# Kernel optimization log

Hardware: AMD Instinct MI355X
Metric: run time of the kernel (lower is better)

## Reference

```python
import jax, jax.numpy as jnp
import numpy as np

N_NODES = 50000
N_EDGES = 600000
D_IN = 128
D_HID = 128
N_IDX = 4096


def gcn_conv(x, W, b, edge_index, num_nodes):
    """PyG GCNConv: add self loops, symmetric deg normalization, scatter-add, bias."""
    h = x @ W  # [N, D_out]
    loop = jnp.arange(num_nodes, dtype=edge_index.dtype)
    src = jnp.concatenate([edge_index[0], loop])
    dst = jnp.concatenate([edge_index[1], loop])
    deg = jax.ops.segment_sum(jnp.ones_like(dst, dtype=h.dtype), dst, num_segments=num_nodes)
    dinv = jnp.where(deg > 0, jax.lax.rsqrt(jnp.maximum(deg, 1.0)), 0.0)
    norm = dinv[src] * dinv[dst]  # [E+N]
    msgs = h[src] * norm[:, None]
    out = jax.ops.segment_sum(msgs, dst, num_segments=num_nodes)
    return out + b


def setup_inputs() -> dict:
    key = jax.random.key(0)
    ks = jax.random.split(key, 18)
    d = {
        "x": jax.random.normal(ks[0], (N_NODES, D_IN), dtype=jnp.float32),
        "syntactic_edge_index": jax.random.randint(ks[1], (2, N_EDGES), 0, N_NODES, dtype=jnp.int32),
        "sequential_edge_index": jax.random.randint(ks[2], (2, N_EDGES), 0, N_NODES, dtype=jnp.int32),
        "semantic_edge_index": jax.random.randint(ks[3], (2, N_EDGES), 0, N_NODES, dtype=jnp.int32),
        "index": jax.random.randint(ks[4], (N_IDX,), 0, N_NODES, dtype=jnp.int32),
    }
    s = 1.0 / np.sqrt(D_IN)
    names = ["syn", "seq", "sem"]
    for i, n in enumerate(names):
        d[f"w1_{n}"] = jax.random.uniform(ks[5 + i], (D_IN, D_HID), jnp.float32, -s, s)
        d[f"b1_{n}"] = jnp.zeros((D_HID,), jnp.float32)
        d[f"w2_{n}"] = jax.random.uniform(ks[8 + i], (D_HID, D_HID), jnp.float32, -s, s)
        d[f"b2_{n}"] = jnp.zeros((D_HID,), jnp.float32)
    return d


def reference(x, syntactic_edge_index, sequential_edge_index, semantic_edge_index, index,
              w1_syn, b1_syn, w1_seq, b1_seq, w1_sem, b1_sem,
              w2_syn, b2_syn, w2_seq, b2_seq, w2_sem, b2_sem):
    n = x.shape[0]
    # layer 1: three parallel GCN branches + ReLU (dropout is identity in eval mode)
    a = jax.nn.relu(gcn_conv(x, w1_syn, b1_syn, syntactic_edge_index, n))
    b = jax.nn.relu(gcn_conv(x, w1_seq, b1_seq, sequential_edge_index, n))
    c = jax.nn.relu(gcn_conv(x, w1_sem, b1_sem, semantic_edge_index, n))
    h = jnp.maximum(jnp.maximum(a, b), c)
    # layer 2
    a2 = jax.nn.relu(gcn_conv(h, w2_syn, b2_syn, syntactic_edge_index, n))
    b2 = jax.nn.relu(gcn_conv(h, w2_seq, b2_seq, sequential_edge_index, n))
    c2 = jax.nn.relu(gcn_conv(h, w2_sem, b2_sem, semantic_edge_index, n))
    out = jnp.maximum(jnp.maximum(a2, b2), c2)
    return out[index]
```

## Files before the change

kernel.cpp:

```cpp
#include <hip/hip_runtime.h>
#include <hip/hip_fp16.h>

#define NN 50000
#define NE 600000
#define NG 3
#define D  128
#define NI 4096
#define BW 1024
#define NBUCK 49
#define EPT_BIN 16
#define EPB_BIN (256 * EPT_BIN)
#define NBLK_BIN ((NE + EPB_BIN - 1) / EPB_BIN)
#define UNR 8

typedef _Float16 half8 __attribute__((ext_vector_type(8)));
typedef float floatx4 __attribute__((ext_vector_type(4)));


__global__ __launch_bounds__(256) void xcvt_kernel(const float* __restrict__ x,
    __half* __restrict__ xh, int n2) {
  int i = blockIdx.x * 256 + threadIdx.x;
  if (i >= n2) return;
  float2 v = ((const float2*)x)[i];
  ((__half2*)xh)[i] = __floats2half2_rn(v.x, v.y);
}

__global__ __launch_bounds__(256) void wcvt_kernel(
    const float* __restrict__ W0, const float* __restrict__ W1, const float* __restrict__ W2,
    const float* __restrict__ W3, const float* __restrict__ W4, const float* __restrict__ W5,
    __half* __restrict__ Wf) {
  const float* Wm[6] = {W0, W1, W2, W3, W4, W5};
  int t = blockIdx.x * 256 + threadIdx.x;
  if (t >= 6 * 2048) return;
  int mat = t >> 11;
  int fr = (t >> 6) & 31;
  int lane = t & 63;
  int tt = fr >> 2, ks = fr & 3;
  int n = tt * 16 + (lane & 15);
  int kb = ks * 32 + (lane >> 4) * 8;
  const float* W = Wm[mat];
#pragma unroll
  for (int j = 0; j < 8; j++)
    Wf[(size_t)t * 8 + j] = __float2half(W[(kb + j) * 128 + n]);
}


__global__ __launch_bounds__(256) void count_kernel(const int* __restrict__ e0,
    const int* __restrict__ e1, const int* __restrict__ e2, int* __restrict__ bucketCnt) {
  __shared__ int cnt[NBUCK];
  int g = blockIdx.y;
  const int* ei = (g == 0) ? e0 : ((g == 1) ? e1 : e2);
  int tid = threadIdx.x;
  if (tid < NBUCK) cnt[tid] = 0;
  __syncthreads();
  int base = blockIdx.x * EPB_BIN;
#pragma unroll
  for (int i = 0; i < EPT_BIN; i++) {
    int e = base + tid + i * 256;
    if (e < NE) atomicAdd(&cnt[ei[NE + e] >> 10], 1);
  }
  __syncthreads();
  if (tid < NBUCK) atomicAdd(&bucketCnt[g * NBUCK + tid], cnt[tid]);
}

__global__ void bscan_kernel(const int* __restrict__ bucketCnt, int* __restrict__ bucketBase,
                             int* __restrict__ cursor, int* __restrict__ rp) {
  int g = threadIdx.x;
  if (g >= NG) return;
  int run = 0;
  for (int b = 0; b < NBUCK; b++) {
    int c = bucketCnt[g * NBUCK + b];
    bucketBase[g * NBUCK + b] = run;
    cursor[g * NBUCK + b] = run;
    run += c;
  }
  rp[g * (NN + 1) + NN] = NE;
}

__global__ __launch_bounds__(256) void bin_kernel(const int* __restrict__ e0,
    const int* __restrict__ e1, const int* __restrict__ e2,
    int* __restrict__ cursor, unsigned int* __restrict__ binned) {
  __shared__ int cnt[NBUCK];
  __shared__ int base[NBUCK];
  int g = blockIdx.y;
  const int* ei = (g == 0) ? e0 : ((g == 1) ? e1 : e2);
  int tid = threadIdx.x;
  if (tid < NBUCK) cnt[tid] = 0;
  __syncthreads();
  int estart = blockIdx.x * EPB_BIN;
  int src[EPT_BIN], dst[EPT_BIN], rk[EPT_BIN];
#pragma unroll
  for (int i = 0; i < EPT_BIN; i++) {
    int e = estart + tid + i * 256;
    if (e < NE) {
      src[i] = ei[e];
      dst[i] = ei[NE + e];
      rk[i] = atomicAdd(&cnt[dst[i] >> 10], 1);
    } else {
      rk[i] = -1;
    }
  }
  __syncthreads();
  if (tid < NBUCK) base[tid] = (cnt[tid] > 0) ? atomicAdd(&cursor[g * NBUCK + tid], cnt[tid]) : 0;
  __syncthreads();
#pragma unroll
  for (int i = 0; i < EPT_BIN; i++) {
    if (rk[i] >= 0) {
      int b = dst[i] >> 10;
      binned[(size_t)g * NE + base[b] + rk[i]] =
          (unsigned int)src[i] | ((unsigned int)dst[i] << 16);
    }
  }
}

__global__ __launch_bounds__(256) void csr_kernel(const unsigned int* __restrict__ binned,
    const int* __restrict__ bucketBase, const int* __restrict__ bucketCnt,
    int* __restrict__ rp, int* __restrict__ col, float* __restrict__ dinv) {
  __shared__ int deg[BW];
  __shared__ int wsum[4];
  int g = blockIdx.y, b = blockIdx.x;
  int tid = threadIdx.x;
  int node0 = b * BW;
  int bb = bucketBase[g * NBUCK + b];
  int total = bucketCnt[g * NBUCK + b];
  const unsigned int* bp = binned + (size_t)g * NE + bb;
  for (int i = tid; i < BW; i += 256) deg[i] = 0;
  __syncthreads();
  for (int e = tid; e < total; e += 256) {
    unsigned int p = bp[e];
    atomicAdd(&deg[(int)(p >> 16) - node0], 1);
  }
  __syncthreads();
  int d0 = deg[tid * 4], d1 = deg[tid * 4 + 1], d2 = deg[tid * 4 + 2], d3 = deg[tid * 4 + 3];
  int s = d0 + d1 + d2 + d3;
  int lane = tid & 63;
  int incl = s;
#pragma unroll
  for (int off = 1; off < 64; off <<= 1) {
    int n = __shfl_up(incl, off, 64);
    if (lane >= off) incl += n;
  }
  if (lane == 63) wsum[tid >> 6] = incl;
  __syncthreads();
  int wbase = 0;
#pragma unroll
  for (int w = 0; w < 4; w++)
    if (w < (tid >> 6)) wbase += wsum[w];
  int ex = wbase + incl - s;
  int exs[4] = {ex, ex + d0, ex + d0 + d1, ex + d0 + d1 + d2};
  int ds[4] = {d0, d1, d2, d3};
#pragma unroll
  for (int k = 0; k < 4; k++) {
    int node = node0 + tid * 4 + k;
    if (node < NN) {
      rp[g * (NN + 1) + node] = bb + exs[k];
      dinv[g * NN + node] = rsqrtf((float)ds[k] + 1.0f);
    }
    deg[tid * 4 + k] = exs[k];
  }
  __syncthreads();
  for (int e = tid; e < total; e += 256) {
    unsigned int p = bp[e];
    int r = atomicAdd(&deg[(int)(p >> 16) - node0], 1);
    col[(size_t)g * NE + bb + r] = (int)(p & 0xffffu);
  }
}


__global__ __launch_bounds__(256) void aggf_kernel(
    const __half* __restrict__ src, const int* __restrict__ rp,
    const int* __restrict__ col, const float* __restrict__ dinv,
    const int* __restrict__ index, __half* __restrict__ tout, int nrows) {
  int w = (blockIdx.x * 256 + threadIdx.x) >> 6;
  if (w >= nrows) return;
  int lane = threadIdx.x & 63;
  int node = index ? index[w] : w;
  int d0 = lane * 2;
  float2 self = __half22float2(*(const __half2*)&src[(size_t)node * D + d0]);
  float di0 = dinv[node];
  float di1 = dinv[NN + node];
  float di2 = dinv[2 * NN + node];
  int s0 = rp[node],                e0 = rp[node + 1];
  int s1 = rp[(NN + 1) + node],     e1 = rp[(NN + 1) + node + 1];
  int s2 = rp[2 * (NN + 1) + node], e2 = rp[2 * (NN + 1) + node + 1];
  int n0 = e0 - s0, n1 = e1 - s1, n2 = e2 - s2;
  int c0 = (lane < n0) ? col[s0 + lane] : 0;
  int c1 = (lane < n1) ? col[NE + s1 + lane] : 0;
  int c2 = (lane < n2) ? col[2 * NE + s2 + lane] : 0;
  float ax0 = di0 * self.x, ay0 = di0 * self.y;
  float ax1 = di1 * self.x, ay1 = di1 * self.y;
  float ax2 = di2 * self.x, ay2 = di2 * self.y;
  int m0 = min(n0, 64), m1 = min(n1, 64), m2 = min(n2, 64);
  int mx = max(m0, max(m1, m2));
  for (int j = 0; j < mx; j += UNR) {
    float2 v0[UNR], v1[UNR], v2[UNR];
    float g0[UNR], g1[UNR], g2[UNR];
#pragma unroll
    for (int k = 0; k < UNR; k++) {
      int jk = j + k;
      int t0 = __shfl(c0, jk, 64); t0 = (jk < m0) ? t0 : node;
      int t1 = __shfl(c1, jk, 64); t1 = (jk < m1) ? t1 : node;
      int t2 = __shfl(c2, jk, 64); t2 = (jk < m2) ? t2 : node;
      g0[k] = (jk < m0) ? dinv[t0] : 0.f;
      g1[k] = (jk < m1) ? dinv[NN + t1] : 0.f;
      g2[k] = (jk < m2) ? dinv[2 * NN + t2] : 0.f;
      v0[k] = __half22float2(*(const __half2*)&src[(size_t)t0 * D + d0]);
      v1[k] = __half22float2(*(const __half2*)&src[(size_t)t1 * D + d0]);
      v2[k] = __half22float2(*(const __half2*)&src[(size_t)t2 * D + d0]);
    }
#pragma unroll
    for (int k = 0; k < UNR; k++) {
      ax0 += g0[k] * v0[k].x; ay0 += g0[k] * v0[k].y;
      ax1 += g1[k] * v1[k].x; ay1 += g1[k] * v1[k].y;
      ax2 += g2[k] * v2[k].x; ay2 += g2[k] * v2[k].y;
    }
  }
  for (int q = s0 + 64; q < e0; q += 64) {
    int nn = min(e0 - q, 64);
    int c = (lane < nn) ? col[q + lane] : 0;
    for (int j = 0; j < nn; j++) {
      int t = __shfl(c, j, 64);
      float g = dinv[t];
      float2 v = __half22float2(*(const __half2*)&src[(size_t)t * D + d0]);
      ax0 += g * v.x; ay0 += g * v.y;
    }
  }
  for (int q = s1 + 64; q < e1; q += 64) {
    int nn = min(e1 - q, 64);
    int c = (lane < nn) ? col[NE + q + lane] : 0;
    for (int j = 0; j < nn; j++) {
      int t = __shfl(c, j, 64);
      float g = dinv[NN + t];
      float2 v = __half22float2(*(const __half2*)&src[(size_t)t * D + d0]);
      ax1 += g * v.x; ay1 += g * v.y;
    }
  }
  for (int q = s2 + 64; q < e2; q += 64) {
    int nn = min(e2 - q, 64);
    int c = (lane < nn) ? col[2 * NE + q + lane] : 0;
    for (int j = 0; j < nn; j++) {
      int t = __shfl(c, j, 64);
      float g = dinv[2 * NN + t];
      float2 v = __half22float2(*(const __half2*)&src[(size_t)t * D + d0]);
      ax2 += g * v.x; ay2 += g * v.y;
    }
  }
  size_t stride = (size_t)nrows * D;
  *(__half2*)&tout[(size_t)w * D + d0]              = __floats2half2_rn(di0 * ax0, di0 * ay0);
  *(__half2*)&tout[stride + (size_t)w * D + d0]     = __floats2half2_rn(di1 * ax1, di1 * ay1);
  *(__half2*)&tout[2 * stride + (size_t)w * D + d0] = __floats2half2_rn(di2 * ax2, di2 * ay2);
}


__global__ __launch_bounds__(256) void mmf_kernel(const __half* __restrict__ A,
    const __half* __restrict__ Wf,
    const float* __restrict__ B0, const float* __restrict__ B1, const float* __restrict__ B2,
    __half* __restrict__ outh, float* __restrict__ outf, int M) {
  __shared__ _Float16 Ws[16384];
  const float* Bb[3] = {B0, B1, B2};
  const int tid = threadIdx.x;
  const int wave = tid >> 6, lane = tid & 63;
  const int wr = (wave >> 1) * 64, wc = (wave & 1) * 64;
  const int ln = lane & 15, quad = lane >> 4;
  const int row_base = blockIdx.x * 128 + wr;
  float om[4][4][4];

  for (int b = 0; b < 3; b++) {
    const __half* Wb = Wf + (size_t)b * 16384;
#pragma unroll
    for (int i = 0; i < 8; i++) {
      int id = tid + i * 256;
      *(half8*)&Ws[id * 8] = *(const half8*)&Wb[(size_t)id * 8];
    }
    __syncthreads();

    const __half* Ab = A + (size_t)b * M * D;
    float bias[4];
#pragma unroll
    for (int ct = 0; ct < 4; ct++) bias[ct] = Bb[b][wc + ct * 16 + ln];
    floatx4 acc[4][4];
#pragma unroll
    for (int rt = 0; rt < 4; rt++)
#pragma unroll
      for (int ct = 0; ct < 4; ct++)
        acc[rt][ct] = (floatx4){bias[ct], bias[ct], bias[ct], bias[ct]};

#pragma unroll
    for (int ks = 0; ks < 4; ks++) {
      half8 av[4];
#pragma unroll
      for (int rt = 0; rt < 4; rt++) {
        int r = row_base + rt * 16 + ln;
        r = (r < M) ? r : (M - 1);
        av[rt] = *(const half8*)&Ab[(size_t)r * D + ks * 32 + quad * 8];
      }
#pragma unroll
      for (int ct = 0; ct < 4; ct++) {
        int tt = (wc >> 4) + ct;
        half8 bv = *(const half8*)&Ws[((tt * 4 + ks) * 64 + lane) * 8];
#pragma unroll
        for (int rt = 0; rt < 4; rt++)
          acc[rt][ct] = __builtin_amdgcn_mfma_f32_16x16x32_f16(av[rt], bv, acc[rt][ct], 0, 0, 0);
      }
    }
#pragma unroll
    for (int rt = 0; rt < 4; rt++)
#pragma unroll
      for (int ct = 0; ct < 4; ct++)
#pragma unroll
        for (int r = 0; r < 4; r++) {
          float v = fmaxf(acc[rt][ct][r], 0.f);
          om[rt][ct][r] = (b == 0) ? v : fmaxf(om[rt][ct][r], v);
        }
    __syncthreads();
  }
#pragma unroll
  for (int rt = 0; rt < 4; rt++) {
    int m = row_base + rt * 16 + quad * 4;
#pragma unroll
    for (int r = 0; r < 4; r++) {
      if (m + r < M) {
#pragma unroll
        for (int ct = 0; ct < 4; ct++) {
          int n = wc + ct * 16 + ln;
          if (outh) outh[(size_t)(m + r) * D + n] = __float2half(om[rt][ct][r]);
          else      outf[(size_t)(m + r) * D + n] = om[rt][ct][r];
        }
      }
    }
  }
}


extern "C" void kernel_launch(void* const* d_in, const int* in_sizes, int n_in,
                              void* d_out, int out_size, void* d_ws, size_t ws_size,
                              hipStream_t stream) {
  const float* x = (const float*)d_in[0];
  const int* e0 = (const int*)d_in[1];
  const int* e1 = (const int*)d_in[2];
  const int* e2 = (const int*)d_in[3];
  const int* index = (const int*)d_in[4];
  const float* w1[3] = {(const float*)d_in[5], (const float*)d_in[9],  (const float*)d_in[13]};
  const float* b1[3] = {(const float*)d_in[6], (const float*)d_in[10], (const float*)d_in[14]};
  const float* w2[3] = {(const float*)d_in[7], (const float*)d_in[11], (const float*)d_in[15]};
  const float* b2[3] = {(const float*)d_in[8], (const float*)d_in[12], (const float*)d_in[16]};
  float* out = (float*)d_out;

  char* ws = (char*)d_ws;
  size_t o = 0;
  auto alloc = [&](size_t bytes) {
    o = (o + 255) & ~(size_t)255;
    void* p = ws + o;
    o += bytes;
    return p;
  };
  int*    rp     = (int*)alloc((size_t)NG * (NN + 1) * 4);
  int*    col    = (int*)alloc((size_t)NG * NE * 4);
  float*  dinv   = (float*)alloc((size_t)NG * NN * 4);
  int*    bcnt   = (int*)alloc((size_t)NG * NBUCK * 4);
  int*    bbase  = (int*)alloc((size_t)NG * NBUCK * 4);
  int*    bcur   = (int*)alloc((size_t)NG * NBUCK * 4);
  __half* xh     = (__half*)alloc((size_t)NN * D * 2);
  __half* Wf     = (__half*)alloc((size_t)6 * 128 * 128 * 2);
  __half* t1     = (__half*)alloc((size_t)NG * NN * D * 2);
  __half* hacc   = (__half*)alloc((size_t)NN * D * 2);
  unsigned int* binned = (unsigned int*)t1;
  __half* t2     = t1;
  (void)ws_size; (void)in_sizes; (void)n_in; (void)out_size;

  hipMemsetAsync(bcnt, 0, (size_t)NG * NBUCK * 4, stream);
  xcvt_kernel<<<(NN * D / 2 + 255) / 256, 256, 0, stream>>>(x, xh, NN * D / 2);
  wcvt_kernel<<<48, 256, 0, stream>>>(w1[0], w1[1], w1[2], w2[0], w2[1], w2[2], Wf);
  count_kernel<<<dim3(NBLK_BIN, NG), 256, 0, stream>>>(e0, e1, e2, bcnt);
  bscan_kernel<<<1, 64, 0, stream>>>(bcnt, bbase, bcur, rp);
  bin_kernel<<<dim3(NBLK_BIN, NG), 256, 0, stream>>>(e0, e1, e2, bcur, binned);
  csr_kernel<<<dim3(NBUCK, NG), 256, 0, stream>>>(binned, bbase, bcnt, rp, col, dinv);

  aggf_kernel<<<(NN * 64 + 255) / 256, 256, 0, stream>>>(xh, rp, col, dinv, nullptr, t1, NN);
  mmf_kernel<<<(NN + 127) / 128, 256, 0, stream>>>(t1, Wf, b1[0], b1[1], b1[2],
                                                   hacc, nullptr, NN);
  aggf_kernel<<<(NI * 64 + 255) / 256, 256, 0, stream>>>(hacc, rp, col, dinv, index, t2, NI);
  mmf_kernel<<<(NI + 127) / 128, 256, 0, stream>>>(t2, Wf + (size_t)3 * 16384,
                                                   b2[0], b2[1], b2[2], nullptr, out, NI);
}
```

Baseline: 312.2 us.

## Pack source dinv weight into CSR entries and split waves into half-wave edge lanes

Splits CSR fill into a separate kernel that stores each edge as a 16-bit source id plus the fp16 source dinv weight, so the gather no longer does a dependent dinv[src] load per edge. The aggregation kernel now has each half-wave handle a different edge with 8-byte half4 loads per lane, covering two edges per step, and combines the halves with a cross-lane xor shuffle at the end. Branch loops are also predicated per branch, so padded iterations no longer load the self row. This adds one kernel launch and rounds the normalization weight to fp16.

```diff
diff --git a/kernel.cpp b/kernel.cpp
--- a/kernel.cpp
+++ b/kernel.cpp
@@ -11,10 +11,24 @@
 #define EPT_BIN 16
 #define EPB_BIN (256 * EPT_BIN)
 #define NBLK_BIN ((NE + EPB_BIN - 1) / EPB_BIN)
-#define UNR 8
 
 typedef _Float16 half8 __attribute__((ext_vector_type(8)));
+typedef _Float16 half4v __attribute__((ext_vector_type(4)));
 typedef float floatx4 __attribute__((ext_vector_type(4)));
+
+static __device__ __forceinline__ float wextract(unsigned int v) {
+  unsigned short u = (unsigned short)(v >> 16);
+  _Float16 h;
+  __builtin_memcpy(&h, &u, 2);
+  return (float)h;
+}
+
+static __device__ __forceinline__ unsigned int packsw(int s, float w) {
+  _Float16 h = (_Float16)w;
+  unsigned short u;
+  __builtin_memcpy(&u, &h, 2);
+  return (unsigned int)s | ((unsigned int)u << 16);
+}
 
 
 __global__ __launch_bounds__(256) void xcvt_kernel(const float* __restrict__ x,
@@ -115,7 +129,7 @@
 
 __global__ __launch_bounds__(256) void csr_kernel(const unsigned int* __restrict__ binned,
     const int* __restrict__ bucketBase, const int* __restrict__ bucketCnt,
-    int* __restrict__ rp, int* __restrict__ col, float* __restrict__ dinv) {
+    int* __restrict__ rp, float* __restrict__ dinv) {
   __shared__ int deg[BW];
   __shared__ int wsum[4];
   int g = blockIdx.y, b = blockIdx.x;
@@ -156,99 +170,162 @@
       rp[g * (NN + 1) + node] = bb + exs[k];
       dinv[g * NN + node] = rsqrtf((float)ds[k] + 1.0f);
     }
-    deg[tid * 4 + k] = exs[k];
+  }
+}
+
+__global__ __launch_bounds__(256) void fillp_kernel(const unsigned int* __restrict__ binned,
+    const int* __restrict__ bucketBase, const int* __restrict__ bucketCnt,
+    const int* __restrict__ rp, const float* __restrict__ dinv,
+    unsigned int* __restrict__ colp) {
+  __shared__ int cur[BW];
+  int g = blockIdx.y, b = blockIdx.x;
+  int tid = threadIdx.x;
+  int node0 = b * BW;
+  int bb = bucketBase[g * NBUCK + b];
+  int total = bucketCnt[g * NBUCK + b];
+  const unsigned int* bp = binned + (size_t)g * NE + bb;
+  for (int i = tid; i < BW; i += 256) {
+    int node = node0 + i;
+    cur[i] = (node < NN) ? rp[g * (NN + 1) + node] : 0;
   }
   __syncthreads();
   for (int e = tid; e < total; e += 256) {
     unsigned int p = bp[e];
-    int r = atomicAdd(&deg[(int)(p >> 16) - node0], 1);
-    col[(size_t)g * NE + bb + r] = (int)(p & 0xffffu);
+    int srcid = (int)(p & 0xffffu);
+    int r = atomicAdd(&cur[(int)(p >> 16) - node0], 1);
+    colp[(size_t)g * NE + r] = packsw(srcid, dinv[g * NN + srcid]);
   }
 }
 
 
 __global__ __launch_bounds__(256) void aggf_kernel(
-    const __half* __restrict__ src, const int* __restrict__ rp,
-    const int* __restrict__ col, const float* __restrict__ dinv,
+    const __half* __restrict__ srch, const int* __restrict__ rp,
+    const unsigned int* __restrict__ colp, const float* __restrict__ dinv,
     const int* __restrict__ index, __half* __restrict__ tout, int nrows) {
   int w = (blockIdx.x * 256 + threadIdx.x) >> 6;
   if (w >= nrows) return;
   int lane = threadIdx.x & 63;
+  int sub = lane >> 5;
+  int fl = lane & 31;
   int node = index ? index[w] : w;
-  int d0 = lane * 2;
-  float2 self = __half22float2(*(const __half2*)&src[(size_t)node * D + d0]);
-  float di0 = dinv[node];
-  float di1 = dinv[NN + node];
-  float di2 = dinv[2 * NN + node];
+  const _Float16* srcv = (const _Float16*)srch;
+  half4v selfh = *(const half4v*)&srcv[(size_t)node * D + fl * 4];
+  float di0 = dinv[node], di1 = dinv[NN + node], di2 = dinv[2 * NN + node];
+  float a0[4], a1[4], a2[4];
+#pragma unroll
+  for (int k = 0; k < 4; k++) {
+    float sv = sub ? 0.f : (float)selfh[k];
+    a0[k] = di0 * sv; a1[k] = di1 * sv; a2[k] = di2 * sv;
+  }
   int s0 = rp[node],                e0 = rp[node + 1];
   int s1 = rp[(NN + 1) + node],     e1 = rp[(NN + 1) + node + 1];
   int s2 = rp[2 * (NN + 1) + node], e2 = rp[2 * (NN + 1) + node + 1];
   int n0 = e0 - s0, n1 = e1 - s1, n2 = e2 - s2;
-  int c0 = (lane < n0) ? col[s0 + lane] : 0;
-  int c1 = (lane < n1) ? col[NE + s1 + lane] : 0;
-  int c2 = (lane < n2) ? col[2 * NE + s2 + lane] : 0;
-  float ax0 = di0 * self.x, ay0 = di0 * self.y;
-  float ax1 = di1 * self.x, ay1 = di1 * self.y;
-  float ax2 = di2 * self.x, ay2 = di2 * self.y;
+  unsigned int c0 = (lane < n0) ? colp[s0 + lane] : 0u;
+  unsigned int c1 = (lane < n1) ? colp[NE + s1 + lane] : 0u;
+  unsigned int c2 = (lane < n2) ? colp[2 * NE + s2 + lane] : 0u;
   int m0 = min(n0, 64), m1 = min(n1, 64), m2 = min(n2, 64);
   int mx = max(m0, max(m1, m2));
-  for (int j = 0; j < mx; j += UNR) {
-    float2 v0[UNR], v1[UNR], v2[UNR];
-    float g0[UNR], g1[UNR], g2[UNR];
-#pragma unroll
-    for (int k = 0; k < UNR; k++) {
-      int jk = j + k;
-      int t0 = __shfl(c0, jk, 64); t0 = (jk < m0) ? t0 : node;
-      int t1 = __shfl(c1, jk, 64); t1 = (jk < m1) ? t1 : node;
-      int t2 = __shfl(c2, jk, 64); t2 = (jk < m2) ? t2 : node;
-      g0[k] = (jk < m0) ? dinv[t0] : 0.f;
-      g1[k] = (jk < m1) ? dinv[NN + t1] : 0.f;
-      g2[k] = (jk < m2) ? dinv[2 * NN + t2] : 0.f;
-      v0[k] = __half22float2(*(const __half2*)&src[(size_t)t0 * D + d0]);
-      v1[k] = __half22float2(*(const __half2*)&src[(size_t)t1 * D + d0]);
-      v2[k] = __half22float2(*(const __half2*)&src[(size_t)t2 * D + d0]);
-    }
-#pragma unroll
-    for (int k = 0; k < UNR; k++) {
-      ax0 += g0[k] * v0[k].x; ay0 += g0[k] * v0[k].y;
-      ax1 += g1[k] * v1[k].x; ay1 += g1[k] * v1[k].y;
-      ax2 += g2[k] * v2[k].x; ay2 += g2[k] * v2[k].y;
+  for (int j = 0; j < mx; j += 8) {
+    half4v h0[4], h1[4], h2[4];
+    float w0[4], w1[4], w2[4];
+    bool p0 = j < m0, p1 = j < m1, p2 = j < m2;
+    if (p0) {
+#pragma unroll
+      for (int u = 0; u < 4; u++) {
+        unsigned int v = (unsigned int)__shfl((int)c0, j + u * 2 + sub, 64);
+        w0[u] = wextract(v);
+        h0[u] = *(const half4v*)&srcv[(size_t)(v & 0xffffu) * D + fl * 4];
+      }
+    }
+    if (p1) {
+#pragma unroll
+      for (int u = 0; u < 4; u++) {
+        unsigned int v = (unsigned int)__shfl((int)c1, j + u * 2 + sub, 64);
+        w1[u] = wextract(v);
+        h1[u] = *(const half4v*)&srcv[(size_t)(v & 0xffffu) * D + fl * 4];
+      }
+    }
+    if (p2) {
+#pragma unroll
+      for (int u = 0; u < 4; u++) {
+        unsigned int v = (unsigned int)__shfl((int)c2, j + u * 2 + sub, 64);
+        w2[u] = wextract(v);
+        h2[u] = *(const half4v*)&srcv[(size_t)(v & 0xffffu) * D + fl * 4];
+      }
+    }
+    if (p0) {
+#pragma unroll
+      for (int u = 0; u < 4; u++)
+#pragma unroll
+        for (int k = 0; k < 4; k++) a0[k] = fmaf((float)h0[u][k], w0[u], a0[k]);
+    }
+    if (p1) {
+#pragma unroll
+      for (int u = 0; u < 4; u++)
+#pragma unroll
+        for (int k = 0; k < 4; k++) a1[k] = fmaf((float)h1[u][k], w1[u], a1[k]);
+    }
+    if (p2) {
+#pragma unroll
+      for (int u = 0; u < 4; u++)
+#pragma unroll
+        for (int k = 0; k < 4; k++) a2[k] = fmaf((float)h2[u][k], w2[u], a2[k]);
     }
   }
   for (int q = s0 + 64; q < e0; q += 64) {
     int nn = min(e0 - q, 64);
-    int c = (lane < nn) ? col[q + lane] : 0;
-    for (int j = 0; j < nn; j++) {
-      int t = __shfl(c, j, 64);
-      float g = dinv[t];
-      float2 v = __half22float2(*(const __half2*)&src[(size_t)t * D + d0]);
-      ax0 += g * v.x; ay0 += g * v.y;
+    unsigned int c = (lane < nn) ? colp[q + lane] : 0u;
+    for (int j = 0; j < nn; j += 2) {
+      unsigned int v = (unsigned int)__shfl((int)c, j + sub, 64);
+      float wf = wextract(v);
+      half4v hv = *(const half4v*)&srcv[(size_t)(v & 0xffffu) * D + fl * 4];
+#pragma unroll
+      for (int k = 0; k < 4; k++) a0[k] = fmaf((float)hv[k], wf, a0[k]);
     }
   }
   for (int q = s1 + 64; q < e1; q += 64) {
     int nn = min(e1 - q, 64);
-    int c = (lane < nn) ? col[NE + q + lane] : 0;
-    for (int j = 0; j < nn; j++) {
-      int t = __shfl(c, j, 64);
-      float g = dinv[NN + t];
-      float2 v = __half22float2(*(const __half2*)&src[(size_t)t * D + d0]);
-      ax1 += g * v.x; ay1 += g * v.y;
+    unsigned int c = (lane < nn) ? colp[NE + q + lane] : 0u;
+    for (int j = 0; j < nn; j += 2) {
+      unsigned int v = (unsigned int)__shfl((int)c, j + sub, 64);
+      float wf = wextract(v);
+      half4v hv = *(const half4v*)&srcv[(size_t)(v & 0xffffu) * D + fl * 4];
+#pragma unroll
+      for (int k = 0; k < 4; k++) a1[k] = fmaf((float)hv[k], wf, a1[k]);
     }
   }
   for (int q = s2 + 64; q < e2; q += 64) {
     int nn = min(e2 - q, 64);
-    int c = (lane < nn) ? col[2 * NE + q + lane] : 0;
-    for (int j = 0; j < nn; j++) {
-      int t = __shfl(c, j, 64);
-      float g = dinv[2 * NN + t];
-      float2 v = __half22float2(*(const __half2*)&src[(size_t)t * D + d0]);
-      ax2 += g * v.x; ay2 += g * v.y;
-    }
-  }
-  size_t stride = (size_t)nrows * D;
-  *(__half2*)&tout[(size_t)w * D + d0]              = __floats2half2_rn(di0 * ax0, di0 * ay0);
-  *(__half2*)&tout[stride + (size_t)w * D + d0]     = __floats2half2_rn(di1 * ax1, di1 * ay1);
-  *(__half2*)&tout[2 * stride + (size_t)w * D + d0] = __floats2half2_rn(di2 * ax2, di2 * ay2);
+    unsigned int c = (lane < nn) ? colp[2 * NE + q + lane] : 0u;
+    for (int j = 0; j < nn; j += 2) {
+      unsigned int v = (unsigned int)__shfl((int)c, j + sub, 64);
+      float wf = wextract(v);
+      half4v hv = *(const half4v*)&srcv[(size_t)(v & 0xffffu) * D + fl * 4];
+#pragma unroll
+      for (int k = 0; k < 4; k++) a2[k] = fmaf((float)hv[k], wf, a2[k]);
+    }
+  }
+#pragma unroll
+  for (int k = 0; k < 4; k++) {
+    a0[k] += __shfl_xor(a0[k], 32, 64);
+    a1[k] += __shfl_xor(a1[k], 32, 64);
+    a2[k] += __shfl_xor(a2[k], 32, 64);
+  }
+  if (sub == 0) {
+    size_t stride = (size_t)nrows * D;
+    _Float16* tv = (_Float16*)tout;
+    half4v o0, o1, o2;
+#pragma unroll
+    for (int k = 0; k < 4; k++) {
+      o0[k] = (_Float16)(di0 * a0[k]);
+      o1[k] = (_Float16)(di1 * a1[k]);
+      o2[k] = (_Float16)(di2 * a2[k]);
+    }
+    *(half4v*)&tv[(size_t)w * D + fl * 4]              = o0;
+    *(half4v*)&tv[stride + (size_t)w * D + fl * 4]     = o1;
+    *(half4v*)&tv[2 * stride + (size_t)w * D + fl * 4] = o2;
+  }
 }
 
 
@@ -355,7 +432,7 @@
     return p;
   };
   int*    rp     = (int*)alloc((size_t)NG * (NN + 1) * 4);
-  int*    col    = (int*)alloc((size_t)NG * NE * 4);
+  unsigned int* colp = (unsigned int*)alloc((size_t)NG * NE * 4);
   float*  dinv   = (float*)alloc((size_t)NG * NN * 4);
   int*    bcnt   = (int*)alloc((size_t)NG * NBUCK * 4);
   int*    bbase  = (int*)alloc((size_t)NG * NBUCK * 4);
@@ -374,12 +451,13 @@
   count_kernel<<<dim3(NBLK_BIN, NG), 256, 0, stream>>>(e0, e1, e2, bcnt);
   bscan_kernel<<<1, 64, 0, stream>>>(bcnt, bbase, bcur, rp);
   bin_kernel<<<dim3(NBLK_BIN, NG), 256, 0, stream>>>(e0, e1, e2, bcur, binned);
-  csr_kernel<<<dim3(NBUCK, NG), 256, 0, stream>>>(binned, bbase, bcnt, rp, col, dinv);
-
-  aggf_kernel<<<(NN * 64 + 255) / 256, 256, 0, stream>>>(xh, rp, col, dinv, nullptr, t1, NN);
+  csr_kernel<<<dim3(NBUCK, NG), 256, 0, stream>>>(binned, bbase, bcnt, rp, dinv);
+  fillp_kernel<<<dim3(NBUCK, NG), 256, 0, stream>>>(binned, bbase, bcnt, rp, dinv, colp);
+
+  aggf_kernel<<<(NN * 64 + 255) / 256, 256, 0, stream>>>(xh, rp, colp, dinv, nullptr, t1, NN);
   mmf_kernel<<<(NN + 127) / 128, 256, 0, stream>>>(t1, Wf, b1[0], b1[1], b1[2],
                                                    hacc, nullptr, NN);
-  aggf_kernel<<<(NI * 64 + 255) / 256, 256, 0, stream>>>(hacc, rp, col, dinv, index, t2, NI);
+  aggf_kernel<<<(NI * 64 + 255) / 256, 256, 0, stream>>>(hacc, rp, colp, dinv, index, t2, NI);
   mmf_kernel<<<(NI + 127) / 128, 256, 0, stream>>>(t2, Wf + (size_t)3 * 16384,
                                                    b2[0], b2[1], b2[2], nullptr, out, NI);
 }
```

New measurement: 297.5 us. 4.7% less time.
